# Optimization experiments

Hardware: AMD Instinct MI355X
Metric: run time of the kernel (lower is better)

The kernel has to match this reference:

```python
import jax, jax.numpy as jnp
import numpy as np

DECAY = 0.5
THRESHOLD = 0.5
ALPHA = 1.0  # triangle surrogate width

@jax.custom_vjp
def spike_fn(v):
    # Heaviside spike on (u - threshold)
    return (v >= 0.0).astype(v.dtype)

def _spike_fwd(v):
    return spike_fn(v), v

def _spike_bwd(v, g):
    # triangle surrogate: max(0, 1 - |v|/a) / a
    return (g * jnp.maximum(0.0, 1.0 - jnp.abs(v) / ALPHA) / ALPHA,)

spike_fn.defvjp(_spike_fwd, _spike_bwd)

def lif_serial(I_seq):
    # I_seq: [T, B, H] input current; serial LIF with hard (multiplicative) reset
    def step(u, I_t):
        u_cur = DECAY * u + I_t
        s = spike_fn(u_cur - THRESHOLD)
        u_next = u_cur * (1.0 - s)
        return u_next, s
    u0 = jnp.zeros(I_seq.shape[1:], dtype=I_seq.dtype)
    _, spikes = jax.lax.scan(step, u0, I_seq)
    return spikes  # [T, B, H]

def setup_inputs() -> dict:
    key = jax.random.key(0)
    ks = jax.random.split(key, 7)
    B, T, D, H = 32, 512, 512, 1024
    x = jax.random.normal(ks[0], (B, T, D), dtype=jnp.float32)
    s_in = 1.0 / np.sqrt(D)
    s_h = 1.0 / np.sqrt(H)
    W0 = jax.random.uniform(ks[1], (H, D), jnp.float32, -s_in, s_in)
    b0 = jax.random.uniform(ks[2], (H,), jnp.float32, -s_in, s_in)
    W1 = jax.random.uniform(ks[3], (H, H), jnp.float32, -s_h, s_h)
    b1 = jax.random.uniform(ks[4], (H,), jnp.float32, -s_h, s_h)
    W2 = jax.random.uniform(ks[5], (H, H), jnp.float32, -s_h, s_h)
    b2 = jax.random.uniform(ks[6], (H,), jnp.float32, -s_h, s_h)
    return {"x": x, "W0": W0, "b0": b0, "W1": W1, "b1": b1, "W2": W2, "b2": b2}

def reference(x, W0, b0, W1, b1, W2, b2):
    # batch_first=True -> transpose to time-major [T, B, D]
    h = jnp.transpose(x, (1, 0, 2))
    for W, b in ((W0, b0), (W1, b1), (W2, b2)):
        h = jnp.einsum('tbd,hd->tbh', h, W) + b  # Linear over all timesteps
        h = lif_serial(h)                         # serial spiking neuron
    return jnp.transpose(h, (1, 0, 2))  # back to [B, T, H]
```

## Files before the change

kernel.cpp:

```cpp
#include <hip/hip_runtime.h>

#define BM 64
#define BN 64
#define BK 16
#define PAD 4

typedef double f64x4 __attribute__((ext_vector_type(4)));
typedef int i32x4 __attribute__((ext_vector_type(4)));
typedef int i32x16 __attribute__((ext_vector_type(16)));

template <typename PT>
__global__ __launch_bounds__(256) void gemm_nt(const float* __restrict__ A,
                                               const float* __restrict__ W,
                                               const float* __restrict__ bias,
                                               PT* __restrict__ C,
                                               int M, int D, int H) {
    __shared__ float As[BK][BM + PAD];
    __shared__ float Ws[BK][BN + PAD];
    const int tid = threadIdx.x;
    const int tx = tid & 15;
    const int ty = tid >> 4;
    const int row0 = blockIdx.x * BM;
    const int col0 = blockIdx.y * BN;
    const int lr = tid >> 2;
    const int lk = (tid & 3) << 2;

    double acc[4][4];
#pragma unroll
    for (int i = 0; i < 4; ++i)
#pragma unroll
        for (int j = 0; j < 4; ++j)
            acc[i][j] = (double)bias[col0 + tx * 4 + j];

    const float* Aptr = A + (size_t)(row0 + lr) * D + lk;
    const float* Wptr = W + (size_t)(col0 + lr) * D + lk;

    for (int kk = 0; kk < D; kk += BK) {
        float4 av = *reinterpret_cast<const float4*>(Aptr + kk);
        float4 wv = *reinterpret_cast<const float4*>(Wptr + kk);
        __syncthreads();
        As[lk + 0][lr] = av.x; As[lk + 1][lr] = av.y;
        As[lk + 2][lr] = av.z; As[lk + 3][lr] = av.w;
        Ws[lk + 0][lr] = wv.x; Ws[lk + 1][lr] = wv.y;
        Ws[lk + 2][lr] = wv.z; Ws[lk + 3][lr] = wv.w;
        __syncthreads();
#pragma unroll
        for (int k = 0; k < BK; ++k) {
            float a[4], w[4];
#pragma unroll
            for (int i = 0; i < 4; ++i) a[i] = As[k][ty * 4 + i];
#pragma unroll
            for (int j = 0; j < 4; ++j) w[j] = Ws[k][tx * 4 + j];
#pragma unroll
            for (int i = 0; i < 4; ++i)
#pragma unroll
                for (int j = 0; j < 4; ++j)
                    acc[i][j] += (double)a[i] * (double)w[j];
        }
    }
#pragma unroll
    for (int i = 0; i < 4; ++i) {
        size_t r = (size_t)(row0 + ty * 4 + i) * H + col0 + tx * 4;
#pragma unroll
        for (int j = 0; j < 4; ++j)
            C[r + j] = (PT)acc[i][j];
    }
}

__global__ __launch_bounds__(256, 4) void gemm_f64mfma(const float* __restrict__ A,
                                                       const float* __restrict__ W,
                                                       const float* __restrict__ bias,
                                                       double* __restrict__ P,
                                                       int M, int D, int H) {
    __shared__ float As[64][36];
    __shared__ float Bs[64][36];
    const int tid = threadIdx.x;
    const int wave = tid >> 6, lane = tid & 63;
    const int l15 = lane & 15, l4 = lane >> 4;
    const int row0 = blockIdx.x * 64, col0 = blockIdx.y * 64;
    const int lrow = tid >> 2;
    const int lk8 = (tid & 3) << 3;

    int rowidx[4];
    {
        double pa = (l4 == 0) ? (double)l15 : 0.0;
        double pb = (l4 == 0) ? 1.0 : 0.0;
        f64x4 pd = {0.0, 0.0, 0.0, 0.0};
        pd = __builtin_amdgcn_mfma_f64_16x16x4f64(pa, pb, pd, 0, 0, 0);
#pragma unroll
        for (int i = 0; i < 4; ++i) rowidx[i] = (int)pd[i];
    }

    f64x4 acc[4];
#pragma unroll
    for (int ct = 0; ct < 4; ++ct) {
        double bv = (double)bias[col0 + ct * 16 + l15];
        acc[ct][0] = bv; acc[ct][1] = bv; acc[ct][2] = bv; acc[ct][3] = bv;
    }

    const float* Aptr = A + (size_t)(row0 + lrow) * D + lk8;
    const float* Wptr = W + (size_t)(col0 + lrow) * D + lk8;

    float4 a0 = *reinterpret_cast<const float4*>(Aptr);
    float4 a1 = *reinterpret_cast<const float4*>(Aptr + 4);
    float4 b0 = *reinterpret_cast<const float4*>(Wptr);
    float4 b1 = *reinterpret_cast<const float4*>(Wptr + 4);

    for (int k0 = 0; k0 < D; k0 += 32) {
        __syncthreads();
        *reinterpret_cast<float4*>(&As[lrow][lk8]) = a0;
        *reinterpret_cast<float4*>(&As[lrow][lk8 + 4]) = a1;
        *reinterpret_cast<float4*>(&Bs[lrow][lk8]) = b0;
        *reinterpret_cast<float4*>(&Bs[lrow][lk8 + 4]) = b1;
        __syncthreads();
        if (k0 + 32 < D) {
            a0 = *reinterpret_cast<const float4*>(Aptr + k0 + 32);
            a1 = *reinterpret_cast<const float4*>(Aptr + k0 + 36);
            b0 = *reinterpret_cast<const float4*>(Wptr + k0 + 32);
            b1 = *reinterpret_cast<const float4*>(Wptr + k0 + 36);
        }
#pragma unroll
        for (int ks = 0; ks < 8; ++ks) {
            double a = (double)As[wave * 16 + l15][ks * 4 + l4];
#pragma unroll
            for (int ct = 0; ct < 4; ++ct) {
                double b = (double)Bs[ct * 16 + l15][ks * 4 + l4];
                acc[ct] = __builtin_amdgcn_mfma_f64_16x16x4f64(a, b, acc[ct], 0, 0, 0);
            }
        }
    }
#pragma unroll
    for (int ct = 0; ct < 4; ++ct) {
#pragma unroll
        for (int i = 0; i < 4; ++i) {
            size_t row = (size_t)(row0 + wave * 16 + rowidx[i]);
            P[row * H + col0 + ct * 16 + l15] = acc[ct][i];
        }
    }
}

__global__ __launch_bounds__(256) void w_decomp(const float* __restrict__ W,
                                                signed char* __restrict__ Wc) {
    const int tid = threadIdx.x;
    const int sub = blockIdx.x * 4 + (tid >> 6);
    const int lane = tid & 63;
    const int h = (sub >> 5) * 32 + (lane & 31);
    const int k = (sub & 31) * 32 + (lane >> 5) * 16;
    const float* wp = W + (size_t)h * 1024 + k;

    int q0[4] = {0, 0, 0, 0}, q1[4] = {0, 0, 0, 0}, q2[4] = {0, 0, 0, 0};
#pragma unroll
    for (int j = 0; j < 16; ++j) {
        int val = (int)lrintf(wp[j] * 134217728.0f);
        int d0 = (int)((unsigned)(val + 128) & 255u) - 128;
        int v1 = (val - d0) >> 8;
        int d1 = (int)((unsigned)(v1 + 128) & 255u) - 128;
        int d2 = (v1 - d1) >> 8;
        q0[j >> 2] |= (d0 & 255) << (8 * (j & 3));
        q1[j >> 2] |= (d1 & 255) << (8 * (j & 3));
        q2[j >> 2] |= (d2 & 255) << (8 * (j & 3));
    }
    const size_t off = (size_t)sub * 1024 + lane * 16;
    int4 o0 = {q0[0], q0[1], q0[2], q0[3]};
    int4 o1 = {q1[0], q1[1], q1[2], q1[3]};
    int4 o2 = {q2[0], q2[1], q2[2], q2[3]};
    *reinterpret_cast<int4*>(Wc + 0 * 1048576 + off) = o0;
    *reinterpret_cast<int4*>(Wc + 1 * 1048576 + off) = o1;
    *reinterpret_cast<int4*>(Wc + 2 * 1048576 + off) = o2;
}

__global__ __launch_bounds__(256, 4) void spike_i8gemm(
    const signed char* __restrict__ S8, const signed char* __restrict__ Wc,
    const float* __restrict__ bias, double* __restrict__ P) {
    const int tid = threadIdx.x;
    const int wave = tid >> 6, lane = tid & 63;
    const int l31 = lane & 31, lg = lane >> 5;
    const int mb = blockIdx.x * 2 + (wave >> 1);
    const int hb = blockIdx.y * 2 + (wave & 1);
    const int m0 = mb * 32, h0 = hb * 32;

    i32x16 c0 = {0, 0, 0, 0, 0, 0, 0, 0, 0, 0, 0, 0, 0, 0, 0, 0};
    i32x16 c1 = c0, c2 = c0;

    const signed char* Ap = S8 + (size_t)mb * 32768 + lane * 16;
    const signed char* Bp = Wc + (size_t)hb * 32768 + lane * 16;

    i32x4 aA  = *reinterpret_cast<const i32x4*>(Ap);
    i32x4 bA0 = *reinterpret_cast<const i32x4*>(Bp);
    i32x4 bA1 = *reinterpret_cast<const i32x4*>(Bp + 1048576);
    i32x4 bA2 = *reinterpret_cast<const i32x4*>(Bp + 2097152);
    i32x4 aB  = *reinterpret_cast<const i32x4*>(Ap + 1024);
    i32x4 bB0 = *reinterpret_cast<const i32x4*>(Bp + 1024);
    i32x4 bB1 = *reinterpret_cast<const i32x4*>(Bp + 1048576 + 1024);
    i32x4 bB2 = *reinterpret_cast<const i32x4*>(Bp + 2097152 + 1024);

#pragma unroll 2
    for (int kb = 0; kb < 32; ++kb) {
        i32x4 aN = {0, 0, 0, 0};
        i32x4 bN0 = aN, bN1 = aN, bN2 = aN;
        if (kb + 2 < 32) {
            const int off = (kb + 2) * 1024;
            aN  = *reinterpret_cast<const i32x4*>(Ap + off);
            bN0 = *reinterpret_cast<const i32x4*>(Bp + off);
            bN1 = *reinterpret_cast<const i32x4*>(Bp + 1048576 + off);
            bN2 = *reinterpret_cast<const i32x4*>(Bp + 2097152 + off);
        }
        c0 = __builtin_amdgcn_mfma_i32_32x32x32_i8(aA, bA0, c0, 0, 0, 0);
        c1 = __builtin_amdgcn_mfma_i32_32x32x32_i8(aA, bA1, c1, 0, 0, 0);
        c2 = __builtin_amdgcn_mfma_i32_32x32x32_i8(aA, bA2, c2, 0, 0, 0);
        aA = aB; bA0 = bB0; bA1 = bB1; bA2 = bB2;
        aB = aN; bB0 = bN0; bB1 = bN1; bB2 = bN2;
    }

    const double bv = (double)bias[h0 + l31];
#pragma unroll
    for (int r = 0; r < 16; ++r) {
        const int row = (r & 3) + 8 * (r >> 2) + 4 * lg;
        double jv = (double)c0[r] + 256.0 * (double)c1[r] + 65536.0 * (double)c2[r];
        P[(size_t)(m0 + row) * 1024 + h0 + l31] = bv + jv * 0x1p-27;
    }
}

__global__ __launch_bounds__(256) void lif_scan_pack(const double* __restrict__ P,
                                                     signed char* __restrict__ S8) {
    const int g = blockIdx.x * 256 + threadIdx.x;
    const int h = g & 1023;
    const int b = g >> 10;
    const size_t base = (size_t)b * 512 * 1024 + h;
    const int hpart = (h >> 5) * 1024 + ((h >> 4) & 1) * 512 + (h & 15);
    signed char* out = S8 + (size_t)b * 16 * 32768 + hpart;
    double u = 0.0;
    for (int t0 = 0; t0 < 512; t0 += 8) {
        double I[8];
#pragma unroll
        for (int j = 0; j < 8; ++j)
            I[j] = P[base + (size_t)(t0 + j) * 1024];
#pragma unroll
        for (int j = 0; j < 8; ++j) {
            u = 0.5 * u + I[j];
            signed char s;
            if (u >= 0.5) { s = 1; u = 0.0; } else { s = 0; }
            const int t = t0 + j;
            out[(size_t)(t >> 5) * 32768 + (t & 31) * 16] = s;
        }
    }
}

template <typename PT>
__global__ __launch_bounds__(256) void lif_scan(const PT* __restrict__ P,
                                                float* __restrict__ S,
                                                int B, int T, int H) {
    const int g = blockIdx.x * blockDim.x + threadIdx.x;
    if (g >= B * H) return;
    const int h = g & (H - 1);
    const int b = g / H;
    const size_t base = (size_t)b * T * H + h;
    double u = 0.0;
    for (int t0 = 0; t0 < T; t0 += 8) {
        double I[8];
#pragma unroll
        for (int j = 0; j < 8; ++j)
            I[j] = (double)P[base + (size_t)(t0 + j) * H];
#pragma unroll
        for (int j = 0; j < 8; ++j) {
            u = 0.5 * u + I[j];
            float s;
            if (u >= 0.5) { s = 1.0f; u = 0.0; } else { s = 0.0f; }
            S[base + (size_t)(t0 + j) * H] = s;
        }
    }
}

extern "C" void kernel_launch(void* const* d_in, const int* in_sizes, int n_in,
                              void* d_out, int out_size, void* d_ws, size_t ws_size,
                              hipStream_t stream) {
    const float* x  = (const float*)d_in[0];
    const float* W0 = (const float*)d_in[1];
    const float* b0 = (const float*)d_in[2];
    const float* W1 = (const float*)d_in[3];
    const float* b1 = (const float*)d_in[4];
    const float* W2 = (const float*)d_in[5];
    const float* b2 = (const float*)d_in[6];

    const int B = 32, T = 512, D0 = 512, H = 1024;
    const int M = B * T;

    float* S = (float*)d_out;

    dim3 gemm_grid(M / BM, H / BN);
    const int scan_blocks = (B * H) / 256;

    const size_t P_bytes = (size_t)M * H * sizeof(double);
    const size_t S8_bytes = (size_t)M * H;
    const size_t Wc_bytes = (size_t)3 * H * H;
    const size_t need_i8 = P_bytes + S8_bytes + Wc_bytes;

    if (ws_size >= need_i8) {
        double* P = (double*)d_ws;
        signed char* S8 = (signed char*)d_ws + P_bytes;
        signed char* Wc = (signed char*)d_ws + P_bytes + S8_bytes;
        dim3 i8_grid(M / 64, H / 64);

        gemm_f64mfma<<<dim3(M / 64, H / 64), 256, 0, stream>>>(x, W0, b0, P, M, D0, H);
        lif_scan_pack<<<scan_blocks, 256, 0, stream>>>(P, S8);

        w_decomp<<<256, 256, 0, stream>>>(W1, Wc);
        spike_i8gemm<<<i8_grid, 256, 0, stream>>>(S8, Wc, b1, P);
        lif_scan_pack<<<scan_blocks, 256, 0, stream>>>(P, S8);

        w_decomp<<<256, 256, 0, stream>>>(W2, Wc);
        spike_i8gemm<<<i8_grid, 256, 0, stream>>>(S8, Wc, b2, P);
        lif_scan<double><<<scan_blocks, 256, 0, stream>>>(P, S, B, T, H);
    } else if (ws_size >= P_bytes) {
        double* P = (double*)d_ws;
        gemm_nt<double><<<gemm_grid, 256, 0, stream>>>(x, W0, b0, P, M, D0, H);
        lif_scan<double><<<scan_blocks, 256, 0, stream>>>(P, S, B, T, H);
        gemm_nt<double><<<gemm_grid, 256, 0, stream>>>(S, W1, b1, P, M, H, H);
        lif_scan<double><<<scan_blocks, 256, 0, stream>>>(P, S, B, T, H);
        gemm_nt<double><<<gemm_grid, 256, 0, stream>>>(S, W2, b2, P, M, H, H);
        lif_scan<double><<<scan_blocks, 256, 0, stream>>>(P, S, B, T, H);
    } else {
        float* P = (float*)d_ws;
        gemm_nt<float><<<gemm_grid, 256, 0, stream>>>(x, W0, b0, P, M, D0, H);
        lif_scan<float><<<scan_blocks, 256, 0, stream>>>(P, S, B, T, H);
        gemm_nt<float><<<gemm_grid, 256, 0, stream>>>(S, W1, b1, P, M, H, H);
        lif_scan<float><<<scan_blocks, 256, 0, stream>>>(P, S, B, T, H);
        gemm_nt<float><<<gemm_grid, 256, 0, stream>>>(S, W2, b2, P, M, H, H);
        lif_scan<float><<<scan_blocks, 256, 0, stream>>>(P, S, B, T, H);
    }
}
```

Before: 539.2 us.

## Replace layer-0 FP64 MFMA GEMM with multi-limb int8 MFMA emulation

```diff
diff --git a/kernel.cpp b/kernel.cpp
--- a/kernel.cpp
+++ b/kernel.cpp
@@ -139,6 +139,156 @@
     }
 }
 
+__global__ __launch_bounds__(256) void x_decomp(const float* __restrict__ X,
+                                                signed char* __restrict__ Xp) {
+    const int tid = threadIdx.x;
+    const int sub = blockIdx.x * 4 + (tid >> 6);
+    const int lane = tid & 63;
+    const int m = (sub >> 4) * 32 + (lane & 31);
+    const int k = (sub & 15) * 32 + (lane >> 5) * 16;
+    const float* xp = X + (size_t)m * 512 + k;
+
+    int q0[4] = {0,0,0,0}, q1[4] = {0,0,0,0}, q2[4] = {0,0,0,0};
+    int q3[4] = {0,0,0,0}, q4[4] = {0,0,0,0}, q5[4] = {0,0,0,0};
+#pragma unroll
+    for (int j = 0; j < 16; ++j) {
+        double xv = (double)xp[j];
+        xv = fmin(fmax(xv, -7.999), 7.999);
+        long long V = llrint(xv * 8796093022208.0);
+        int d;
+        d = (int)(((unsigned long long)(V + 128)) & 255ull) - 128; V = (V - d) >> 8;
+        q0[j >> 2] |= (d & 255) << (8 * (j & 3));
+        d = (int)(((unsigned long long)(V + 128)) & 255ull) - 128; V = (V - d) >> 8;
+        q1[j >> 2] |= (d & 255) << (8 * (j & 3));
+        d = (int)(((unsigned long long)(V + 128)) & 255ull) - 128; V = (V - d) >> 8;
+        q2[j >> 2] |= (d & 255) << (8 * (j & 3));
+        d = (int)(((unsigned long long)(V + 128)) & 255ull) - 128; V = (V - d) >> 8;
+        q3[j >> 2] |= (d & 255) << (8 * (j & 3));
+        d = (int)(((unsigned long long)(V + 128)) & 255ull) - 128; V = (V - d) >> 8;
+        q4[j >> 2] |= (d & 255) << (8 * (j & 3));
+        d = (int)V;
+        q5[j >> 2] |= (d & 255) << (8 * (j & 3));
+    }
+    const size_t off = (size_t)sub * 1024 + lane * 16;
+    const size_t PS = 8388608;
+    int4 o;
+    o = {q0[0],q0[1],q0[2],q0[3]}; *reinterpret_cast<int4*>(Xp + 0*PS + off) = o;
+    o = {q1[0],q1[1],q1[2],q1[3]}; *reinterpret_cast<int4*>(Xp + 1*PS + off) = o;
+    o = {q2[0],q2[1],q2[2],q2[3]}; *reinterpret_cast<int4*>(Xp + 2*PS + off) = o;
+    o = {q3[0],q3[1],q3[2],q3[3]}; *reinterpret_cast<int4*>(Xp + 3*PS + off) = o;
+    o = {q4[0],q4[1],q4[2],q4[3]}; *reinterpret_cast<int4*>(Xp + 4*PS + off) = o;
+    o = {q5[0],q5[1],q5[2],q5[3]}; *reinterpret_cast<int4*>(Xp + 5*PS + off) = o;
+}
+
+__global__ __launch_bounds__(256) void w0_decomp(const float* __restrict__ W,
+                                                 signed char* __restrict__ Wp) {
+    const int tid = threadIdx.x;
+    const int sub = blockIdx.x * 4 + (tid >> 6);
+    const int lane = tid & 63;
+    const int h = (sub >> 4) * 32 + (lane & 31);
+    const int k = (sub & 15) * 32 + (lane >> 5) * 16;
+    const float* wp = W + (size_t)h * 512 + k;
+
+    int q0[4] = {0,0,0,0}, q1[4] = {0,0,0,0}, q2[4] = {0,0,0,0};
+    int q3[4] = {0,0,0,0}, q4[4] = {0,0,0,0};
+#pragma unroll
+    for (int j = 0; j < 16; ++j) {
+        long long V = llrint((double)wp[j] * 8796093022208.0);
+        int d;
+        d = (int)(((unsigned long long)(V + 128)) & 255ull) - 128; V = (V - d) >> 8;
+        q0[j >> 2] |= (d & 255) << (8 * (j & 3));
+        d = (int)(((unsigned long long)(V + 128)) & 255ull) - 128; V = (V - d) >> 8;
+        q1[j >> 2] |= (d & 255) << (8 * (j & 3));
+        d = (int)(((unsigned long long)(V + 128)) & 255ull) - 128; V = (V - d) >> 8;
+        q2[j >> 2] |= (d & 255) << (8 * (j & 3));
+        d = (int)(((unsigned long long)(V + 128)) & 255ull) - 128; V = (V - d) >> 8;
+        q3[j >> 2] |= (d & 255) << (8 * (j & 3));
+        d = (int)V;
+        q4[j >> 2] |= (d & 255) << (8 * (j & 3));
+    }
+    const size_t off = (size_t)sub * 1024 + lane * 16;
+    const size_t PS = 524288;
+    int4 o;
+    o = {q0[0],q0[1],q0[2],q0[3]}; *reinterpret_cast<int4*>(Wp + 0*PS + off) = o;
+    o = {q1[0],q1[1],q1[2],q1[3]}; *reinterpret_cast<int4*>(Wp + 1*PS + off) = o;
+    o = {q2[0],q2[1],q2[2],q2[3]}; *reinterpret_cast<int4*>(Wp + 2*PS + off) = o;
+    o = {q3[0],q3[1],q3[2],q3[3]}; *reinterpret_cast<int4*>(Wp + 3*PS + off) = o;
+    o = {q4[0],q4[1],q4[2],q4[3]}; *reinterpret_cast<int4*>(Wp + 4*PS + off) = o;
+}
+
+__global__ __launch_bounds__(256, 2) void gemm_i8L0(
+    const signed char* __restrict__ Xp, const signed char* __restrict__ Wp,
+    const float* __restrict__ bias, double* __restrict__ P) {
+    const int tid = threadIdx.x;
+    const int wave = tid >> 6, lane = tid & 63;
+    const int l31 = lane & 31, lg = lane >> 5;
+    const int mb = blockIdx.x * 2 + (wave >> 1);
+    const int hb = blockIdx.y * 2 + (wave & 1);
+    const int m0 = mb * 32, h0 = hb * 32;
+
+    i32x16 c4 = {0,0,0,0,0,0,0,0,0,0,0,0,0,0,0,0};
+    i32x16 c5 = c4, c6 = c4, c7 = c4, c8 = c4, c9 = c4;
+
+    const size_t AP = 8388608, BP = 524288;
+    const signed char* Ap = Xp + (size_t)mb * 16384 + lane * 16;
+    const signed char* Bp = Wp + (size_t)hb * 16384 + lane * 16;
+
+#define LD_A(p, o) (*reinterpret_cast<const i32x4*>(Ap + (size_t)(p) * AP + (o)))
+#define LD_B(p, o) (*reinterpret_cast<const i32x4*>(Bp + (size_t)(p) * BP + (o)))
+
+    i32x4 a0 = LD_A(0, 0), a1 = LD_A(1, 0), a2 = LD_A(2, 0);
+    i32x4 a3 = LD_A(3, 0), a4 = LD_A(4, 0), a5 = LD_A(5, 0);
+    i32x4 b0 = LD_B(0, 0), b1 = LD_B(1, 0), b2 = LD_B(2, 0);
+    i32x4 b3 = LD_B(3, 0), b4 = LD_B(4, 0);
+
+    for (int kb = 0; kb < 16; ++kb) {
+        i32x4 na0 = {0,0,0,0}, na1 = na0, na2 = na0, na3 = na0, na4 = na0, na5 = na0;
+        i32x4 nb0 = na0, nb1 = na0, nb2 = na0, nb3 = na0, nb4 = na0;
+        if (kb + 1 < 16) {
+            const int off = (kb + 1) * 1024;
+            na0 = LD_A(0, off); na1 = LD_A(1, off); na2 = LD_A(2, off);
+            na3 = LD_A(3, off); na4 = LD_A(4, off); na5 = LD_A(5, off);
+            nb0 = LD_B(0, off); nb1 = LD_B(1, off); nb2 = LD_B(2, off);
+            nb3 = LD_B(3, off); nb4 = LD_B(4, off);
+        }
+        c4 = __builtin_amdgcn_mfma_i32_32x32x32_i8(a0, b4, c4, 0, 0, 0);
+        c4 = __builtin_amdgcn_mfma_i32_32x32x32_i8(a1, b3, c4, 0, 0, 0);
+        c4 = __builtin_amdgcn_mfma_i32_32x32x32_i8(a2, b2, c4, 0, 0, 0);
+        c4 = __builtin_amdgcn_mfma_i32_32x32x32_i8(a3, b1, c4, 0, 0, 0);
+        c4 = __builtin_amdgcn_mfma_i32_32x32x32_i8(a4, b0, c4, 0, 0, 0);
+        c5 = __builtin_amdgcn_mfma_i32_32x32x32_i8(a1, b4, c5, 0, 0, 0);
+        c5 = __builtin_amdgcn_mfma_i32_32x32x32_i8(a2, b3, c5, 0, 0, 0);
+        c5 = __builtin_amdgcn_mfma_i32_32x32x32_i8(a3, b2, c5, 0, 0, 0);
+        c5 = __builtin_amdgcn_mfma_i32_32x32x32_i8(a4, b1, c5, 0, 0, 0);
+        c5 = __builtin_amdgcn_mfma_i32_32x32x32_i8(a5, b0, c5, 0, 0, 0);
+        c6 = __builtin_amdgcn_mfma_i32_32x32x32_i8(a2, b4, c6, 0, 0, 0);
+        c6 = __builtin_amdgcn_mfma_i32_32x32x32_i8(a3, b3, c6, 0, 0, 0);
+        c6 = __builtin_amdgcn_mfma_i32_32x32x32_i8(a4, b2, c6, 0, 0, 0);
+        c6 = __builtin_amdgcn_mfma_i32_32x32x32_i8(a5, b1, c6, 0, 0, 0);
+        c7 = __builtin_amdgcn_mfma_i32_32x32x32_i8(a3, b4, c7, 0, 0, 0);
+        c7 = __builtin_amdgcn_mfma_i32_32x32x32_i8(a4, b3, c7, 0, 0, 0);
+        c7 = __builtin_amdgcn_mfma_i32_32x32x32_i8(a5, b2, c7, 0, 0, 0);
+        c8 = __builtin_amdgcn_mfma_i32_32x32x32_i8(a4, b4, c8, 0, 0, 0);
+        c8 = __builtin_amdgcn_mfma_i32_32x32x32_i8(a5, b3, c8, 0, 0, 0);
+        c9 = __builtin_amdgcn_mfma_i32_32x32x32_i8(a5, b4, c9, 0, 0, 0);
+
+        a0 = na0; a1 = na1; a2 = na2; a3 = na3; a4 = na4; a5 = na5;
+        b0 = nb0; b1 = nb1; b2 = nb2; b3 = nb3; b4 = nb4;
+    }
+#undef LD_A
+#undef LD_B
+
+    const double bv = (double)bias[h0 + l31];
+#pragma unroll
+    for (int r = 0; r < 16; ++r) {
+        const int row = (r & 3) + 8 * (r >> 2) + 4 * lg;
+        double jv = (double)c4[r] * 0x1p-54 + (double)c5[r] * 0x1p-46
+                  + (double)c6[r] * 0x1p-38 + (double)c7[r] * 0x1p-30
+                  + (double)c8[r] * 0x1p-22 + (double)c9[r] * 0x1p-14;
+        P[(size_t)(m0 + row) * 1024 + h0 + l31] = bv + jv;
+    }
+}
+
 __global__ __launch_bounds__(256) void w_decomp(const float* __restrict__ W,
                                                 signed char* __restrict__ Wc) {
     const int tid = threadIdx.x;
@@ -293,7 +443,10 @@
     const size_t P_bytes = (size_t)M * H * sizeof(double);
     const size_t S8_bytes = (size_t)M * H;
     const size_t Wc_bytes = (size_t)3 * H * H;
+    const size_t X6_bytes = (size_t)6 * M * D0;
+    const size_t W5_bytes = (size_t)5 * H * D0;
     const size_t need_i8 = P_bytes + S8_bytes + Wc_bytes;
+    const size_t need_L0 = P_bytes + X6_bytes + W5_bytes;
 
     if (ws_size >= need_i8) {
         double* P = (double*)d_ws;
@@ -301,7 +454,15 @@
         signed char* Wc = (signed char*)d_ws + P_bytes + S8_bytes;
         dim3 i8_grid(M / 64, H / 64);
 
-        gemm_f64mfma<<<dim3(M / 64, H / 64), 256, 0, stream>>>(x, W0, b0, P, M, D0, H);
+        if (ws_size >= need_L0) {
+            signed char* X6 = (signed char*)d_ws + P_bytes;
+            signed char* W5 = (signed char*)d_ws + P_bytes + X6_bytes;
+            x_decomp<<<2048, 256, 0, stream>>>(x, X6);
+            w0_decomp<<<128, 256, 0, stream>>>(W0, W5);
+            gemm_i8L0<<<dim3(M / 64, H / 64), 256, 0, stream>>>(X6, W5, b0, P);
+        } else {
+            gemm_f64mfma<<<dim3(M / 64, H / 64), 256, 0, stream>>>(x, W0, b0, P, M, D0, H);
+        }
         lif_scan_pack<<<scan_blocks, 256, 0, stream>>>(P, S8);
 
         w_decomp<<<256, 256, 0, stream>>>(W1, Wc);
```

After: 470.6 us. 12.7% less time.
